# Optimization experiments

Measured on AMD Instinct MI355X. Metric: run time of the kernel, lower is better.

## Reference

```python
import jax, jax.numpy as jnp
import numpy as np


def setup_inputs() -> dict:
    key = jax.random.key(0)
    B, N = 4, 32768
    xyz = jax.random.normal(key, (B, N, 3), dtype=jnp.float32)
    return {"xyz": xyz, "K": 16, "nqueries": 2048}


def reference(xyz, K, nqueries):
    # xyz: (b, n, 3). Deterministic strided pick of nqueries query points
    # (stand-in for the KD-tree's distance-pick sampling), then brute-force KNN.
    b, n, _ = xyz.shape
    stride = n // nqueries
    q_idx = jnp.arange(nqueries) * stride          # (nq,)
    pts = xyz[:, q_idx, :]                          # (b, nq, 3) sampled query points
    # pairwise squared distances (b, nq, n)
    d = jnp.sum((pts[:, :, None, :] - xyz[:, None, :, :]) ** 2, axis=-1)
    _, idx = jax.lax.top_k(-d, K)                   # (b, nq, K) nearest-neighbor indices
    idx = idx.astype(jnp.int64)[..., None]          # (b, nq, K, 1) matches expand_dims(..., 3)
    return idx, pts
```

## Files before the change

### kernel.cpp

```cpp
#include <hip/hip_runtime.h>
#include <stdint.h>

#define NPTS  32768
#define NQ    2048
#define KNN   16
#define NB    4
#define BLOCK 256
#define WPB   4
#define PPL   8
#define ITERS (NPTS / (64 * PPL))
#define GATE_MARGIN 5e-4f

typedef float f32x2 __attribute__((ext_vector_type(2)));

__device__ __forceinline__ int dpp_shr1_i(int x) {
    return __builtin_amdgcn_update_dpp(x, x, 0x111, 0xf, 0xf, false);
}
__device__ __forceinline__ float dpp_shr1_f(float x) {
    return __int_as_float(dpp_shr1_i(__float_as_int(x)));
}
__device__ __forceinline__ float readlane_f(float x, int l) {
    return __int_as_float(__builtin_amdgcn_readlane(__float_as_int(x), l));
}

__device__ __forceinline__ f32x2 pk_mul(f32x2 a, f32x2 b) {
    f32x2 d;
    asm("v_pk_mul_f32 %0, %1, %2" : "=v"(d) : "v"(a), "v"(b));
    return d;
}
__device__ __forceinline__ f32x2 pk_fma(f32x2 a, f32x2 b, f32x2 c) {
    f32x2 d;
    asm("v_pk_fma_f32 %0, %1, %2, %3" : "=v"(d) : "v"(a), "v"(b), "v"(c));
    return d;
}

template <int T>
__device__ __forceinline__ void insert_all(float d, int p, int lane,
                                           float& ld, int& li, float& tau,
                                           float& th, float qnm)
{
    unsigned long long rem = __ballot(d <= tau);
    while (rem) {
        const int srcl = __ffsll(rem) - 1;
        const float wd = readlane_f(d, srcl);
        const int   wi = __builtin_amdgcn_readlane(p, srcl);
        const bool less = (ld < wd) || (ld == wd && li < wi);
        const unsigned long long lm = __ballot(less);
        const int pos = __popc((unsigned)((lm >> (16 * T)) & 0xffffull));
        const float pld = dpp_shr1_f(ld);
        const int   pli = dpp_shr1_i(li);
        if ((lane >> 4) == T) {
            const int gl = lane & 15;
            if (gl == pos)      { ld = wd;  li = wi;  }
            else if (gl > pos)  { ld = pld; li = pli; }
        }
        tau = readlane_f(ld, 16 * T + 15);
        th  = tau + qnm;
        rem &= rem - 1;
        if (rem) rem &= __ballot(d <= tau);
    }
}

__global__ __launch_bounds__(256) void repack_soa(const float* __restrict__ xyz,
                                                  float* __restrict__ ws)
{
    const int i = blockIdx.x * 256 + threadIdx.x;
    const int b = i / (NPTS / 4);
    const int g = i % (NPTS / 4);
    const float4* src = (const float4*)(xyz + (size_t)b * NPTS * 3) + 3 * g;
    const float4 c0 = src[0], c1 = src[1], c2 = src[2];
    float* xs = ws + (size_t)b * 3 * NPTS;
    float* ys = xs + NPTS;
    float* zs = ys + NPTS;
    ((float4*)xs)[g] = make_float4(c0.x, c0.w, c1.z, c2.y);
    ((float4*)ys)[g] = make_float4(c0.y, c1.x, c1.w, c2.z);
    ((float4*)zs)[g] = make_float4(c0.z, c1.y, c2.x, c2.w);
}

struct PtBuf { float4 x0, x1, y0, y1, z0, z1; };

__device__ __forceinline__ void loadbuf(PtBuf& b, const float* xs,
                                        const float* ys, const float* zs,
                                        unsigned o)
{
    b.x0 = *(const float4*)(xs + o);  b.x1 = *(const float4*)(xs + o + 4);
    b.y0 = *(const float4*)(ys + o);  b.y1 = *(const float4*)(ys + o + 4);
    b.z0 = *(const float4*)(zs + o);  b.z1 = *(const float4*)(zs + o + 4);
}

__device__ __forceinline__ void step_soa(const PtBuf& c, int pb, int lane,
                                         f32x2 M2X0, f32x2 M2Y0, f32x2 M2Z0,
                                         f32x2 M2X1, f32x2 M2Y1, f32x2 M2Z1,
                                         float qx0, float qy0, float qz0,
                                         float qx1, float qy1, float qz1,
                                         float& ld, int& li,
                                         float& tau0, float& tau1,
                                         float& th0, float& th1,
                                         float qnm0, float qnm1)
{
    f32x2 X[4] = { {c.x0.x, c.x0.y}, {c.x0.z, c.x0.w},
                   {c.x1.x, c.x1.y}, {c.x1.z, c.x1.w} };
    f32x2 Y[4] = { {c.y0.x, c.y0.y}, {c.y0.z, c.y0.w},
                   {c.y1.x, c.y1.y}, {c.y1.z, c.y1.w} };
    f32x2 Z[4] = { {c.z0.x, c.z0.y}, {c.z0.z, c.z0.w},
                   {c.z1.x, c.z1.y}, {c.z1.z, c.z1.w} };

    unsigned long long m0[PPL], m1[PPL], any = 0;
    #pragma unroll
    for (int u = 0; u < 4; ++u) {
        const f32x2 s  = pk_fma(Z[u], Z[u], pk_fma(Y[u], Y[u], pk_mul(X[u], X[u])));
        const f32x2 t0 = pk_fma(Z[u], M2Z0, pk_fma(Y[u], M2Y0, pk_fma(X[u], M2X0, s)));
        const f32x2 t1 = pk_fma(Z[u], M2Z1, pk_fma(Y[u], M2Y1, pk_fma(X[u], M2X1, s)));
        m0[2*u]   = __ballot(t0.x <= th0);
        m0[2*u+1] = __ballot(t0.y <= th0);
        m1[2*u]   = __ballot(t1.x <= th1);
        m1[2*u+1] = __ballot(t1.y <= th1);
        any |= m0[2*u] | m0[2*u+1] | m1[2*u] | m1[2*u+1];
    }
    if (any) {
        #pragma unroll
        for (int j = 0; j < PPL; ++j) {
            if (m0[j]) {
                const float pxj = (j & 1) ? X[j >> 1].y : X[j >> 1].x;
                const float pyj = (j & 1) ? Y[j >> 1].y : Y[j >> 1].x;
                const float pzj = (j & 1) ? Z[j >> 1].y : Z[j >> 1].x;
                const float dx = __fadd_rn(pxj, -qx0);
                const float dy = __fadd_rn(pyj, -qy0);
                const float dz = __fadd_rn(pzj, -qz0);
                const float d  = __fadd_rn(
                    __fadd_rn(__fmul_rn(dx, dx), __fmul_rn(dy, dy)),
                    __fmul_rn(dz, dz));
                insert_all<0>(d, pb + j, lane, ld, li, tau0, th0, qnm0);
            }
        }
        #pragma unroll
        for (int j = 0; j < PPL; ++j) {
            if (m1[j]) {
                const float pxj = (j & 1) ? X[j >> 1].y : X[j >> 1].x;
                const float pyj = (j & 1) ? Y[j >> 1].y : Y[j >> 1].x;
                const float pzj = (j & 1) ? Z[j >> 1].y : Z[j >> 1].x;
                const float dx = __fadd_rn(pxj, -qx1);
                const float dy = __fadd_rn(pyj, -qy1);
                const float dz = __fadd_rn(pzj, -qz1);
                const float d  = __fadd_rn(
                    __fadd_rn(__fmul_rn(dx, dx), __fmul_rn(dy, dy)),
                    __fmul_rn(dz, dz));
                insert_all<1>(d, pb + j, lane, ld, li, tau1, th1, qnm1);
            }
        }
    }
}

__global__ __launch_bounds__(BLOCK) void knn_soa(const float* __restrict__ ws,
                                                 float* __restrict__ out_idx,
                                                 float* __restrict__ out_pts)
{
    const int tid  = threadIdx.x;
    const int lane = tid & 63;
    const int wv   = tid >> 6;
    const int w    = blockIdx.x * WPB + wv;
    const int b    = w >> 10;
    const int pr   = w & 1023;
    const float* xs = ws + (size_t)b * 3 * NPTS;
    const float* ys = xs + NPTS;
    const float* zs = ys + NPTS;

    const int qp0 = pr << 5;
    const float qx0 = xs[qp0],      qy0 = ys[qp0],      qz0 = zs[qp0];
    const float qx1 = xs[qp0 + 16], qy1 = ys[qp0 + 16], qz1 = zs[qp0 + 16];

    const int g0 = b * NQ + (pr << 1);
    if (lane == 0) {
        out_pts[3 * g0 + 0] = qx0;
        out_pts[3 * g0 + 1] = qy0;
        out_pts[3 * g0 + 2] = qz0;
        out_pts[3 * g0 + 3] = qx1;
        out_pts[3 * g0 + 4] = qy1;
        out_pts[3 * g0 + 5] = qz1;
    }

    const f32x2 M2X0 = { -2.0f * qx0, -2.0f * qx0 };
    const f32x2 M2Y0 = { -2.0f * qy0, -2.0f * qy0 };
    const f32x2 M2Z0 = { -2.0f * qz0, -2.0f * qz0 };
    const f32x2 M2X1 = { -2.0f * qx1, -2.0f * qx1 };
    const f32x2 M2Y1 = { -2.0f * qy1, -2.0f * qy1 };
    const f32x2 M2Z1 = { -2.0f * qz1, -2.0f * qz1 };
    const float qnm0 = -(qx0 * qx0 + qy0 * qy0 + qz0 * qz0) + GATE_MARGIN;
    const float qnm1 = -(qx1 * qx1 + qy1 * qy1 + qz1 * qz1) + GATE_MARGIN;

    float ld = __builtin_inff();  int li = 0x7fffffff;
    float tau0 = __builtin_inff(), tau1 = __builtin_inff();
    float th0  = __builtin_inff(), th1  = __builtin_inff();

    unsigned o = 8 * (unsigned)lane;

    PtBuf A, Bf;
    loadbuf(A, xs, ys, zs, o);
    int pb = PPL * lane;
    for (int k = 0; k < ITERS; k += 2) {
        loadbuf(Bf, xs, ys, zs, o + 512);
        step_soa(A, pb, lane, M2X0, M2Y0, M2Z0, M2X1, M2Y1, M2Z1,
                 qx0, qy0, qz0, qx1, qy1, qz1,
                 ld, li, tau0, tau1, th0, th1, qnm0, qnm1);
        if (k + 2 < ITERS)
            loadbuf(A, xs, ys, zs, o + 1024);
        step_soa(Bf, pb + 512, lane, M2X0, M2Y0, M2Z0, M2X1, M2Y1, M2Z1,
                 qx0, qy0, qz0, qx1, qy1, qz1,
                 ld, li, tau0, tau1, th0, th1, qnm0, qnm1);
        o += 1024;
        pb += 1024;
    }

    if (lane < 2 * KNN) {
        out_idx[(size_t)g0 * KNN + lane] = (float)li;
    }
}

__device__ __forceinline__ void load6(float4 dst[6], const float4* p) {
    #pragma unroll
    for (int t = 0; t < 6; ++t) dst[t] = p[t];
}

__device__ __forceinline__ void step2(const float4 c[6], int pb, int lane,
                                      float m2x0, float m2y0, float m2z0,
                                      float m2x1, float m2y1, float m2z1,
                                      float qx0, float qy0, float qz0,
                                      float qx1, float qy1, float qz1,
                                      float& ld, int& li,
                                      float& tau0, float& tau1,
                                      float& th0, float& th1,
                                      float qnm0, float qnm1)
{
    float px[PPL], py[PPL], pz[PPL];
    px[0] = c[0].x; py[0] = c[0].y; pz[0] = c[0].z;
    px[1] = c[0].w; py[1] = c[1].x; pz[1] = c[1].y;
    px[2] = c[1].z; py[2] = c[1].w; pz[2] = c[2].x;
    px[3] = c[2].y; py[3] = c[2].z; pz[3] = c[2].w;
    px[4] = c[3].x; py[4] = c[3].y; pz[4] = c[3].z;
    px[5] = c[3].w; py[5] = c[4].x; pz[5] = c[4].y;
    px[6] = c[4].z; py[6] = c[4].w; pz[6] = c[5].x;
    px[7] = c[5].y; py[7] = c[5].z; pz[7] = c[5].w;

    unsigned long long m0[PPL], m1[PPL], any = 0;
    #pragma unroll
    for (int j = 0; j < PPL; ++j) {
        const float s = __fmaf_rn(pz[j], pz[j],
                          __fmaf_rn(py[j], py[j], __fmul_rn(px[j], px[j])));
        float t0 = __fmaf_rn(px[j], m2x0, s);
        t0 = __fmaf_rn(py[j], m2y0, t0);
        t0 = __fmaf_rn(pz[j], m2z0, t0);
        m0[j] = __ballot(t0 <= th0);
        float t1 = __fmaf_rn(px[j], m2x1, s);
        t1 = __fmaf_rn(py[j], m2y1, t1);
        t1 = __fmaf_rn(pz[j], m2z1, t1);
        m1[j] = __ballot(t1 <= th1);
        any |= m0[j] | m1[j];
    }
    if (any) {
        #pragma unroll
        for (int j = 0; j < PPL; ++j) {
            if (m0[j]) {
                const float dx = __fadd_rn(px[j], -qx0);
                const float dy = __fadd_rn(py[j], -qy0);
                const float dz = __fadd_rn(pz[j], -qz0);
                const float d  = __fadd_rn(
                    __fadd_rn(__fmul_rn(dx, dx), __fmul_rn(dy, dy)),
                    __fmul_rn(dz, dz));
                insert_all<0>(d, pb + j, lane, ld, li, tau0, th0, qnm0);
            }
        }
        #pragma unroll
        for (int j = 0; j < PPL; ++j) {
            if (m1[j]) {
                const float dx = __fadd_rn(px[j], -qx1);
                const float dy = __fadd_rn(py[j], -qy1);
                const float dz = __fadd_rn(pz[j], -qz1);
                const float d  = __fadd_rn(
                    __fadd_rn(__fmul_rn(dx, dx), __fmul_rn(dy, dy)),
                    __fmul_rn(dz, dz));
                insert_all<1>(d, pb + j, lane, ld, li, tau1, th1, qnm1);
            }
        }
    }
}

__global__ __launch_bounds__(BLOCK) void knn_aos(const float* __restrict__ xyz,
                                                 float* __restrict__ out_idx,
                                                 float* __restrict__ out_pts)
{
    const int tid  = threadIdx.x;
    const int lane = tid & 63;
    const int wv   = tid >> 6;
    const int w    = blockIdx.x * WPB + wv;
    const int b    = w >> 10;
    const int pr   = w & 1023;
    const size_t base = (size_t)b * NPTS * 3;

    const int qp0 = pr << 5;
    const float qx0 = xyz[base + 3 * qp0 + 0];
    const float qy0 = xyz[base + 3 * qp0 + 1];
    const float qz0 = xyz[base + 3 * qp0 + 2];
    const float qx1 = xyz[base + 3 * qp0 + 48];
    const float qy1 = xyz[base + 3 * qp0 + 49];
    const float qz1 = xyz[base + 3 * qp0 + 50];

    const int g0 = b * NQ + (pr << 1);
    if (lane == 0) {
        out_pts[3 * g0 + 0] = qx0;
        out_pts[3 * g0 + 1] = qy0;
        out_pts[3 * g0 + 2] = qz0;
        out_pts[3 * g0 + 3] = qx1;
        out_pts[3 * g0 + 4] = qy1;
        out_pts[3 * g0 + 5] = qz1;
    }

    const float m2x0 = -2.0f * qx0, m2y0 = -2.0f * qy0, m2z0 = -2.0f * qz0;
    const float m2x1 = -2.0f * qx1, m2y1 = -2.0f * qy1, m2z1 = -2.0f * qz1;
    const float qnm0 = -(qx0 * qx0 + qy0 * qy0 + qz0 * qz0) + GATE_MARGIN;
    const float qnm1 = -(qx1 * qx1 + qy1 * qy1 + qz1 * qz1) + GATE_MARGIN;

    float ld = __builtin_inff();  int li = 0x7fffffff;
    float tau0 = __builtin_inff(), tau1 = __builtin_inff();
    float th0  = __builtin_inff(), th1  = __builtin_inff();

    const float4* lp = (const float4*)(xyz + base) + 6 * lane;

    float4 A[6], Bf[6];
    load6(A, lp);
    for (int k = 0; k < ITERS; k += 2) {
        load6(Bf, lp + 384);
        step2(A, (k << 9) + PPL * lane, lane,
              m2x0, m2y0, m2z0, m2x1, m2y1, m2z1,
              qx0, qy0, qz0, qx1, qy1, qz1,
              ld, li, tau0, tau1, th0, th1, qnm0, qnm1);
        if (k + 2 < ITERS)
            load6(A, lp + 768);
        step2(Bf, ((k + 1) << 9) + PPL * lane, lane,
              m2x0, m2y0, m2z0, m2x1, m2y1, m2z1,
              qx0, qy0, qz0, qx1, qy1, qz1,
              ld, li, tau0, tau1, th0, th1, qnm0, qnm1);
        lp += 768;
    }

    if (lane < 2 * KNN) {
        out_idx[(size_t)g0 * KNN + lane] = (float)li;
    }
}

extern "C" void kernel_launch(void* const* d_in, const int* in_sizes, int n_in,
                              void* d_out, int out_size, void* d_ws, size_t ws_size,
                              hipStream_t stream) {
    const float* xyz = (const float*)d_in[0];
    float* out = (float*)d_out;
    float* out_idx = out;
    float* out_pts = out + (size_t)NB * NQ * KNN;

    const size_t ws_needed = (size_t)NB * 3 * NPTS * sizeof(float);
    const int blocks = (NB * NQ / 2) / WPB;
    if (d_ws != nullptr && ws_size >= ws_needed) {
        float* wsp = (float*)d_ws;
        repack_soa<<<NB * NPTS / 4 / 256, 256, 0, stream>>>(xyz, wsp);
        knn_soa<<<blocks, BLOCK, 0, stream>>>(wsp, out_idx, out_pts);
    } else {
        knn_aos<<<blocks, BLOCK, 0, stream>>>(xyz, out_idx, out_pts);
    }
}
```

Measured before the change: 185.1 us.

## Split KNN scan across two waves with four queries each and shared-threshold gating

```diff
diff --git a/kernel.cpp b/kernel.cpp
--- a/kernel.cpp
+++ b/kernel.cpp
@@ -5,10 +5,9 @@
 #define NQ    2048
 #define KNN   16
 #define NB    4
-#define BLOCK 256
-#define WPB   4
 #define PPL   8
-#define ITERS (NPTS / (64 * PPL))
+#define HALF  (NPTS / 2)
+#define ITERS_H (HALF / (64 * PPL))
 #define GATE_MARGIN 5e-4f
 
 typedef float f32x2 __attribute__((ext_vector_type(2)));
@@ -34,10 +33,9 @@
     return d;
 }
 
-template <int T>
-__device__ __forceinline__ void insert_all(float d, int p, int lane,
-                                           float& ld, int& li, float& tau,
-                                           float& th, float qnm)
+__device__ __forceinline__ void insert_rt(int T, float d, int p, int lane,
+                                          float& ld, int& li, float& tau,
+                                          float& th, float qnm, float ts)
 {
     unsigned long long rem = __ballot(d <= tau);
     while (rem) {
@@ -55,7 +53,7 @@
             else if (gl > pos)  { ld = pld; li = pli; }
         }
         tau = readlane_f(ld, 16 * T + 15);
-        th  = tau + qnm;
+        th  = fminf(tau, ts) + qnm;
         rem &= rem - 1;
         if (rem) rem &= __ballot(d <= tau);
     }
@@ -88,15 +86,14 @@
     b.z0 = *(const float4*)(zs + o);  b.z1 = *(const float4*)(zs + o + 4);
 }
 
-__device__ __forceinline__ void step_soa(const PtBuf& c, int pb, int lane,
-                                         f32x2 M2X0, f32x2 M2Y0, f32x2 M2Z0,
-                                         f32x2 M2X1, f32x2 M2Y1, f32x2 M2Z1,
-                                         float qx0, float qy0, float qz0,
-                                         float qx1, float qy1, float qz1,
-                                         float& ld, int& li,
-                                         float& tau0, float& tau1,
-                                         float& th0, float& th1,
-                                         float qnm0, float qnm1)
+__device__ __forceinline__ void step4(const PtBuf& c, int pb, int lane,
+                                      const f32x2* M2X, const f32x2* M2Y,
+                                      const f32x2* M2Z,
+                                      const float* qx, const float* qy,
+                                      const float* qz,
+                                      float& ld, int& li,
+                                      float* tau, float* th,
+                                      const float* qnm, const float* ts)
 {
     f32x2 X[4] = { {c.x0.x, c.x0.y}, {c.x0.z, c.x0.w},
                    {c.x1.x, c.x1.y}, {c.x1.z, c.x1.w} };
@@ -104,117 +101,147 @@
                    {c.y1.x, c.y1.y}, {c.y1.z, c.y1.w} };
     f32x2 Z[4] = { {c.z0.x, c.z0.y}, {c.z0.z, c.z0.w},
                    {c.z1.x, c.z1.y}, {c.z1.z, c.z1.w} };
-
-    unsigned long long m0[PPL], m1[PPL], any = 0;
-    #pragma unroll
-    for (int u = 0; u < 4; ++u) {
-        const f32x2 s  = pk_fma(Z[u], Z[u], pk_fma(Y[u], Y[u], pk_mul(X[u], X[u])));
-        const f32x2 t0 = pk_fma(Z[u], M2Z0, pk_fma(Y[u], M2Y0, pk_fma(X[u], M2X0, s)));
-        const f32x2 t1 = pk_fma(Z[u], M2Z1, pk_fma(Y[u], M2Y1, pk_fma(X[u], M2X1, s)));
-        m0[2*u]   = __ballot(t0.x <= th0);
-        m0[2*u+1] = __ballot(t0.y <= th0);
-        m1[2*u]   = __ballot(t1.x <= th1);
-        m1[2*u+1] = __ballot(t1.y <= th1);
-        any |= m0[2*u] | m0[2*u+1] | m1[2*u] | m1[2*u+1];
-    }
-    if (any) {
-        #pragma unroll
-        for (int j = 0; j < PPL; ++j) {
-            if (m0[j]) {
-                const float pxj = (j & 1) ? X[j >> 1].y : X[j >> 1].x;
-                const float pyj = (j & 1) ? Y[j >> 1].y : Y[j >> 1].x;
-                const float pzj = (j & 1) ? Z[j >> 1].y : Z[j >> 1].x;
-                const float dx = __fadd_rn(pxj, -qx0);
-                const float dy = __fadd_rn(pyj, -qy0);
-                const float dz = __fadd_rn(pzj, -qz0);
-                const float d  = __fadd_rn(
-                    __fadd_rn(__fmul_rn(dx, dx), __fmul_rn(dy, dy)),
-                    __fmul_rn(dz, dz));
-                insert_all<0>(d, pb + j, lane, ld, li, tau0, th0, qnm0);
+    f32x2 S[4];
+    #pragma unroll
+    for (int u = 0; u < 4; ++u)
+        S[u] = pk_fma(Z[u], Z[u], pk_fma(Y[u], Y[u], pk_mul(X[u], X[u])));
+
+    #pragma unroll
+    for (int t = 0; t < 4; ++t) {
+        unsigned long long m[PPL], any = 0;
+        f32x2 T0[4];
+        #pragma unroll
+        for (int u = 0; u < 4; ++u) {
+            T0[u] = pk_fma(Z[u], M2Z[t],
+                      pk_fma(Y[u], M2Y[t], pk_fma(X[u], M2X[t], S[u])));
+            m[2*u]   = __ballot(T0[u].x <= th[t]);
+            m[2*u+1] = __ballot(T0[u].y <= th[t]);
+            any |= m[2*u] | m[2*u+1];
+        }
+        if (any) {
+            #pragma unroll
+            for (int j = 0; j < PPL; ++j) {
+                if (m[j]) {
+                    const float pxj = (j & 1) ? X[j >> 1].y : X[j >> 1].x;
+                    const float pyj = (j & 1) ? Y[j >> 1].y : Y[j >> 1].x;
+                    const float pzj = (j & 1) ? Z[j >> 1].y : Z[j >> 1].x;
+                    const float dx = __fadd_rn(pxj, -qx[t]);
+                    const float dy = __fadd_rn(pyj, -qy[t]);
+                    const float dz = __fadd_rn(pzj, -qz[t]);
+                    const float d  = __fadd_rn(
+                        __fadd_rn(__fmul_rn(dx, dx), __fmul_rn(dy, dy)),
+                        __fmul_rn(dz, dz));
+                    insert_rt(t, d, pb + j, lane, ld, li,
+                              tau[t], th[t], qnm[t], ts[t]);
+                }
             }
         }
-        #pragma unroll
-        for (int j = 0; j < PPL; ++j) {
-            if (m1[j]) {
-                const float pxj = (j & 1) ? X[j >> 1].y : X[j >> 1].x;
-                const float pyj = (j & 1) ? Y[j >> 1].y : Y[j >> 1].x;
-                const float pzj = (j & 1) ? Z[j >> 1].y : Z[j >> 1].x;
-                const float dx = __fadd_rn(pxj, -qx1);
-                const float dy = __fadd_rn(pyj, -qy1);
-                const float dz = __fadd_rn(pzj, -qz1);
-                const float d  = __fadd_rn(
-                    __fadd_rn(__fmul_rn(dx, dx), __fmul_rn(dy, dy)),
-                    __fmul_rn(dz, dz));
-                insert_all<1>(d, pb + j, lane, ld, li, tau1, th1, qnm1);
-            }
-        }
-    }
-}
-
-__global__ __launch_bounds__(BLOCK) void knn_soa(const float* __restrict__ ws,
-                                                 float* __restrict__ out_idx,
-                                                 float* __restrict__ out_pts)
+    }
+}
+
+__global__ __launch_bounds__(128) void knn4(const float* __restrict__ ws,
+                                            float* __restrict__ out_idx,
+                                            float* __restrict__ out_pts)
 {
     const int tid  = threadIdx.x;
     const int lane = tid & 63;
-    const int wv   = tid >> 6;
-    const int w    = blockIdx.x * WPB + wv;
-    const int b    = w >> 10;
-    const int pr   = w & 1023;
+    const int h    = tid >> 6;
+    const int p    = blockIdx.x;
+    const int b    = p >> 9;
+    const int gg   = p & 511;
     const float* xs = ws + (size_t)b * 3 * NPTS;
     const float* ys = xs + NPTS;
     const float* zs = ys + NPTS;
 
-    const int qp0 = pr << 5;
-    const float qx0 = xs[qp0],      qy0 = ys[qp0],      qz0 = zs[qp0];
-    const float qx1 = xs[qp0 + 16], qy1 = ys[qp0 + 16], qz1 = zs[qp0 + 16];
-
-    const int g0 = b * NQ + (pr << 1);
+    float qx[4], qy[4], qz[4], qnm[4], tau[4], th[4], ts[4];
+    f32x2 M2X[4], M2Y[4], M2Z[4];
+    #pragma unroll
+    for (int t = 0; t < 4; ++t) {
+        const int qp = (gg << 6) + (t << 4);
+        qx[t] = xs[qp]; qy[t] = ys[qp]; qz[t] = zs[qp];
+        M2X[t] = f32x2{ -2.0f * qx[t], -2.0f * qx[t] };
+        M2Y[t] = f32x2{ -2.0f * qy[t], -2.0f * qy[t] };
+        M2Z[t] = f32x2{ -2.0f * qz[t], -2.0f * qz[t] };
+        qnm[t] = -(qx[t]*qx[t] + qy[t]*qy[t] + qz[t]*qz[t]) + GATE_MARGIN;
+        tau[t] = __builtin_inff(); th[t] = __builtin_inff();
+        ts[t]  = __builtin_inff();
+    }
+
+    const int qb = b * NQ + (gg << 2);
+    if (h == 0 && lane == 0) {
+        #pragma unroll
+        for (int t = 0; t < 4; ++t) {
+            out_pts[3 * (qb + t) + 0] = qx[t];
+            out_pts[3 * (qb + t) + 1] = qy[t];
+            out_pts[3 * (qb + t) + 2] = qz[t];
+        }
+    }
+
+    __shared__ float stau[2][4];
     if (lane == 0) {
-        out_pts[3 * g0 + 0] = qx0;
-        out_pts[3 * g0 + 1] = qy0;
-        out_pts[3 * g0 + 2] = qz0;
-        out_pts[3 * g0 + 3] = qx1;
-        out_pts[3 * g0 + 4] = qy1;
-        out_pts[3 * g0 + 5] = qz1;
-    }
-
-    const f32x2 M2X0 = { -2.0f * qx0, -2.0f * qx0 };
-    const f32x2 M2Y0 = { -2.0f * qy0, -2.0f * qy0 };
-    const f32x2 M2Z0 = { -2.0f * qz0, -2.0f * qz0 };
-    const f32x2 M2X1 = { -2.0f * qx1, -2.0f * qx1 };
-    const f32x2 M2Y1 = { -2.0f * qy1, -2.0f * qy1 };
-    const f32x2 M2Z1 = { -2.0f * qz1, -2.0f * qz1 };
-    const float qnm0 = -(qx0 * qx0 + qy0 * qy0 + qz0 * qz0) + GATE_MARGIN;
-    const float qnm1 = -(qx1 * qx1 + qy1 * qy1 + qz1 * qz1) + GATE_MARGIN;
+        stau[h][0] = __builtin_inff(); stau[h][1] = __builtin_inff();
+        stau[h][2] = __builtin_inff(); stau[h][3] = __builtin_inff();
+    }
+    __syncthreads();
 
     float ld = __builtin_inff();  int li = 0x7fffffff;
-    float tau0 = __builtin_inff(), tau1 = __builtin_inff();
-    float th0  = __builtin_inff(), th1  = __builtin_inff();
-
-    unsigned o = 8 * (unsigned)lane;
+
+    unsigned o = h * HALF + 8 * (unsigned)lane;
+    int pb = (int)o;
 
     PtBuf A, Bf;
     loadbuf(A, xs, ys, zs, o);
-    int pb = PPL * lane;
-    for (int k = 0; k < ITERS; k += 2) {
+    for (int k = 0; k < ITERS_H; k += 2) {
         loadbuf(Bf, xs, ys, zs, o + 512);
-        step_soa(A, pb, lane, M2X0, M2Y0, M2Z0, M2X1, M2Y1, M2Z1,
-                 qx0, qy0, qz0, qx1, qy1, qz1,
-                 ld, li, tau0, tau1, th0, th1, qnm0, qnm1);
-        if (k + 2 < ITERS)
+        step4(A, pb, lane, M2X, M2Y, M2Z, qx, qy, qz, ld, li, tau, th, qnm, ts);
+        if (lane == 0) {
+            stau[h][0] = tau[0]; stau[h][1] = tau[1];
+            stau[h][2] = tau[2]; stau[h][3] = tau[3];
+        }
+        #pragma unroll
+        for (int t = 0; t < 4; ++t) {
+            ts[t] = stau[h ^ 1][t];
+            th[t] = fminf(tau[t], ts[t]) + qnm[t];
+        }
+        if (k + 2 < ITERS_H)
             loadbuf(A, xs, ys, zs, o + 1024);
-        step_soa(Bf, pb + 512, lane, M2X0, M2Y0, M2Z0, M2X1, M2Y1, M2Z1,
-                 qx0, qy0, qz0, qx1, qy1, qz1,
-                 ld, li, tau0, tau1, th0, th1, qnm0, qnm1);
+        step4(Bf, pb + 512, lane, M2X, M2Y, M2Z, qx, qy, qz, ld, li, tau, th, qnm, ts);
+        if (lane == 0) {
+            stau[h][0] = tau[0]; stau[h][1] = tau[1];
+            stau[h][2] = tau[2]; stau[h][3] = tau[3];
+        }
+        #pragma unroll
+        for (int t = 0; t < 4; ++t) {
+            ts[t] = stau[h ^ 1][t];
+            th[t] = fminf(tau[t], ts[t]) + qnm[t];
+        }
         o += 1024;
         pb += 1024;
     }
 
-    if (lane < 2 * KNN) {
-        out_idx[(size_t)g0 * KNN + lane] = (float)li;
-    }
-}
+    __shared__ float sd[2 * 64];
+    __shared__ int   si[2 * 64];
+    sd[h * 64 + lane] = ld;
+    si[h * 64 + lane] = li;
+    __syncthreads();
+    const int T  = lane >> 4;
+    const int r  = lane & 15;
+    const int pb2 = (h ^ 1) * 64 + (T << 4);
+    int cnt = 0;
+    #pragma unroll
+    for (int t = 0; t < 16; ++t) {
+        const float od = sd[pb2 + t];
+        const int   oi = si[pb2 + t];
+        cnt += (od < ld || (od == ld && oi < li)) ? 1 : 0;
+    }
+    const int pos = r + cnt;
+    if (pos < KNN)
+        out_idx[(size_t)(qb + T) * KNN + pos] = (float)li;
+}
+
+#define BLOCK 256
+#define WPB   4
+#define ITERS (NPTS / (64 * PPL))
 
 __device__ __forceinline__ void load6(float4 dst[6], const float4* p) {
     #pragma unroll
@@ -266,7 +293,8 @@
                 const float d  = __fadd_rn(
                     __fadd_rn(__fmul_rn(dx, dx), __fmul_rn(dy, dy)),
                     __fmul_rn(dz, dz));
-                insert_all<0>(d, pb + j, lane, ld, li, tau0, th0, qnm0);
+                insert_rt(0, d, pb + j, lane, ld, li, tau0, th0, qnm0,
+                          __builtin_inff());
             }
         }
         #pragma unroll
@@ -278,7 +306,8 @@
                 const float d  = __fadd_rn(
                     __fadd_rn(__fmul_rn(dx, dx), __fmul_rn(dy, dy)),
                     __fmul_rn(dz, dz));
-                insert_all<1>(d, pb + j, lane, ld, li, tau1, th1, qnm1);
+                insert_rt(1, d, pb + j, lane, ld, li, tau1, th1, qnm1,
+                          __builtin_inff());
             }
         }
     }
@@ -356,12 +385,11 @@
     float* out_pts = out + (size_t)NB * NQ * KNN;
 
     const size_t ws_needed = (size_t)NB * 3 * NPTS * sizeof(float);
-    const int blocks = (NB * NQ / 2) / WPB;
     if (d_ws != nullptr && ws_size >= ws_needed) {
         float* wsp = (float*)d_ws;
         repack_soa<<<NB * NPTS / 4 / 256, 256, 0, stream>>>(xyz, wsp);
-        knn_soa<<<blocks, BLOCK, 0, stream>>>(wsp, out_idx, out_pts);
+        knn4<<<NB * NQ / 4, 128, 0, stream>>>(wsp, out_idx, out_pts);
     } else {
-        knn_aos<<<blocks, BLOCK, 0, stream>>>(xyz, out_idx, out_pts);
-    }
-}
+        knn_aos<<<(NB * NQ / 2) / WPB, BLOCK, 0, stream>>>(xyz, out_idx, out_pts);
+    }
+}
```

After: 244.8 us. 1.32x slower.
